# Optimization experiments

Measured on AMD Instinct MI355X. Metric: run time of the kernel, lower is better.

Reference implementation:

```python
import jax, jax.numpy as jnp
import numpy as np
import math

B, H, S, D = 2, 16, 2048, 64
MASK_NEG = -1e9


def setup_inputs() -> dict:
    key = jax.random.key(0)
    kq, kk, kv, kc, km = jax.random.split(key, 5)
    q = jax.random.normal(kq, (B, H, S, D), dtype=jnp.float32)
    k = jax.random.normal(kk, (B, H, S, D), dtype=jnp.float32)
    v = jax.random.normal(kv, (B, H, S, D), dtype=jnp.float32)
    constant = jax.random.normal(kc, (1, H, 1, 1), dtype=jnp.float32)
    mask = jax.random.randint(km, (B, S), 0, 2, dtype=jnp.int32)  # 1 = masked out
    return {"q": q, "k": k, "v": v, "constant": constant, "mask": mask}


def leaky_softmax(x, leaky_factor):
    # custom 'leaky' softmax: denominator gets an extra exp(c - max) * S term
    m = jnp.max(x, axis=-1, keepdims=True)
    exp_x = jnp.exp(x - m)
    leak = jnp.exp(leaky_factor - m) * x.shape[-1]
    return exp_x / (jnp.sum(exp_x, axis=-1, keepdims=True) + leak)


def reference(q, k, v, constant, mask):
    scale = jnp.float32(1.0 / math.sqrt(q.shape[-1]))
    # scores: [B,H,S,S]
    scores = jnp.einsum("bhqd,bhkd->bhqk", q, k) * scale
    m = mask.astype(q.dtype)[:, None, None, :]  # [B,1,1,S]
    scores = scores + m * MASK_NEG
    probs = leaky_softmax(scores, constant)
    out = jnp.einsum("bhqk,bhkd->bhqd", probs, v)
    return out, probs
```

## Files before the change

kernel.cpp:

```cpp
#include <hip/hip_runtime.h>
#include <hip/hip_bf16.h>
#include <cstdint>
#include <cstddef>

#define BB 2
#define HH 16
#define SS 2048
#define DD 64
#define NBH (BB * HH)
#define BQ 16
#define NWAVES 8
#define BLK 512
#define CW 512
#define NCHUNK (SS / CW)
#define CSTRIDE 516

typedef __attribute__((ext_vector_type(8))) short bf16x8;
typedef __attribute__((ext_vector_type(4))) float f32x4;
typedef __attribute__((ext_vector_type(4))) unsigned short us4;

#define LGKM_BAR() asm volatile("s_waitcnt lgkmcnt(0)\n\ts_barrier" ::: "memory")

__device__ __forceinline__ unsigned short f2bf(float x) {
  union { float f; uint32_t u; } c;
  c.f = x;
  uint32_t u = c.u;
  uint32_t r = (u + 0x7FFFu + ((u >> 16) & 1u)) >> 16;
  return (unsigned short)r;
}

__global__ __launch_bounds__(256) void cvt_qk_kernel(
    const float* __restrict__ q, const float* __restrict__ k,
    unsigned short* __restrict__ qb, unsigned short* __restrict__ kb) {
  size_t i = ((size_t)blockIdx.x * 256 + threadIdx.x) * 4;
  float4 a = *(const float4*)(q + i);
  float4 b = *(const float4*)(k + i);
  us4 qa = {f2bf(a.x), f2bf(a.y), f2bf(a.z), f2bf(a.w)};
  us4 ka = {f2bf(b.x), f2bf(b.y), f2bf(b.z), f2bf(b.w)};
  *(us4*)(qb + i) = qa;
  *(us4*)(kb + i) = ka;
}

__global__ __launch_bounds__(256) void cvt_vt_kernel(
    const float* __restrict__ v, unsigned short* __restrict__ vt) {
  __shared__ unsigned short t[64][65];
  const int tid = threadIdx.x;
  const int bh = blockIdx.y;
  const int s0 = blockIdx.x * 64;
  const float* vb = v + ((size_t)bh * SS + s0) * DD;
#pragma unroll
  for (int it = 0; it < 16; ++it) {
    int idx = it * 256 + tid;
    int s = idx >> 6, d = idx & 63;
    t[s][d] = f2bf(vb[idx]);
  }
  __syncthreads();
  unsigned short* vo = vt + (size_t)bh * DD * SS + s0;
#pragma unroll
  for (int it = 0; it < 4; ++it) {
    int idx = it * 256 + tid;
    int d = idx >> 4;
    int s4 = (idx & 15) * 4;
    us4 w = {t[s4 + 0][d], t[s4 + 1][d], t[s4 + 2][d], t[s4 + 3][d]};
    *(us4*)(vo + (size_t)d * SS + s4) = w;
  }
}

__global__ __launch_bounds__(BLK, 2) void attn_kernel(
    const unsigned short* __restrict__ qb,
    const unsigned short* __restrict__ kb,
    const unsigned short* __restrict__ vt,
    const float* __restrict__ cst,
    const int* __restrict__ mask,
    float* __restrict__ out,
    float* __restrict__ probs) {
  __shared__ float pch[BQ][CSTRIDE];
  __shared__ float stats[NWAVES][BQ];
  __shared__ float rowinv[BQ];

  const int tid = threadIdx.x;
  const int wave = tid >> 6;
  const int lane = tid & 63;
  const int quad = lane >> 4;
  const int l16 = lane & 15;
  const int bh = blockIdx.y;
  const int bidx = bh >> 4;
  const int h = bh & 15;
  const int q0 = blockIdx.x * BQ;

  const unsigned short* qrow = qb + ((size_t)bh * SS + q0 + l16) * DD + quad * 8;
  bf16x8 aq0 = *(const bf16x8*)(qrow);
  bf16x8 aq1 = *(const bf16x8*)(qrow + 32);

  const unsigned short* kbase = kb + (size_t)bh * SS * DD;
  f32x4 acc[16];
#pragma unroll
  for (int t = 0; t < 16; ++t) {
    int col0 = (wave + 8 * t) * 16;
    const unsigned short* krow = kbase + (size_t)(col0 + l16) * DD + quad * 8;
    bf16x8 bk0 = *(const bf16x8*)(krow);
    bf16x8 bk1 = *(const bf16x8*)(krow + 32);
    f32x4 c = {0.f, 0.f, 0.f, 0.f};
    c = __builtin_amdgcn_mfma_f32_16x16x32_bf16(aq0, bk0, c, 0, 0, 0);
    c = __builtin_amdgcn_mfma_f32_16x16x32_bf16(aq1, bk1, c, 0, 0, 0);
    acc[t] = c;
  }

  float rsum[4] = {0.f, 0.f, 0.f, 0.f};
#pragma unroll
  for (int t = 0; t < 16; ++t) {
    int col = (wave + 8 * t) * 16 + l16;
    int mk = mask[bidx * SS + col];
#pragma unroll
    for (int r = 0; r < 4; ++r) {
      float e = mk ? 0.0f : __expf(acc[t][r] * 0.125f);
      acc[t][r] = e;
      rsum[r] += e;
    }
  }
#pragma unroll
  for (int off = 8; off >= 1; off >>= 1)
#pragma unroll
    for (int r = 0; r < 4; ++r)
      rsum[r] += __shfl_xor(rsum[r], off, 64);
  if (l16 == 0)
#pragma unroll
    for (int r = 0; r < 4; ++r) stats[wave][quad * 4 + r] = rsum[r];
  __syncthreads();
  if (tid < BQ) {
    float s = 0.f;
#pragma unroll
    for (int w = 0; w < NWAVES; ++w) s += stats[w][tid];
    float denom = s + __expf(cst[h]) * (float)SS;
    rowinv[tid] = 1.0f / denom;
  }
  __syncthreads();
  float inv[4];
#pragma unroll
  for (int r = 0; r < 4; ++r) inv[r] = rowinv[quad * 4 + r];

  f32x4 acco[4];
#pragma unroll
  for (int dt = 0; dt < 4; ++dt) acco[dt] = (f32x4){0.f, 0.f, 0.f, 0.f};
  const unsigned short* vbase = vt + (size_t)bh * DD * SS;
#pragma unroll
  for (int c = 0; c < NCHUNK; ++c) {
    const int kg0 = c * CW + wave * 64 + quad * 8;
    bf16x8 v0[4];
#pragma unroll
    for (int dt = 0; dt < 4; ++dt)
      v0[dt] = *(const bf16x8*)(vbase + (size_t)(dt * 16 + l16) * SS + kg0);

    if (c) LGKM_BAR();
#pragma unroll
    for (int tt = 0; tt < 4; ++tt) {
      int t = c * 4 + tt;
      int lcol = tt * 128 + wave * 16 + l16;
#pragma unroll
      for (int r = 0; r < 4; ++r)
        pch[quad * 4 + r][lcol] = acc[t][r] * inv[r];
    }
    LGKM_BAR();

    {
      const f32x4* ap4 = (const f32x4*)&pch[l16][wave * 64 + quad * 8];
      f32x4 p0 = ap4[0], p1 = ap4[1];
      union { bf16x8 v8; uint32_t u[4]; } apu;
      asm("v_cvt_pk_bf16_f32 %0, %1, %2" : "=v"(apu.u[0]) : "v"(p0.x), "v"(p0.y));
      asm("v_cvt_pk_bf16_f32 %0, %1, %2" : "=v"(apu.u[1]) : "v"(p0.z), "v"(p0.w));
      asm("v_cvt_pk_bf16_f32 %0, %1, %2" : "=v"(apu.u[2]) : "v"(p1.x), "v"(p1.y));
      asm("v_cvt_pk_bf16_f32 %0, %1, %2" : "=v"(apu.u[3]) : "v"(p1.z), "v"(p1.w));
      bf16x8 ap = apu.v8;
      bf16x8 v1[4];
#pragma unroll
      for (int dt = 0; dt < 4; ++dt)
        v1[dt] = *(const bf16x8*)(vbase + (size_t)(dt * 16 + l16) * SS + kg0 + 32);
#pragma unroll
      for (int dt = 0; dt < 4; ++dt)
        acco[dt] = __builtin_amdgcn_mfma_f32_16x16x32_bf16(ap, v0[dt], acco[dt], 0, 0, 0);

      const f32x4* bp4 = (const f32x4*)&pch[l16][wave * 64 + 32 + quad * 8];
      f32x4 q0v = bp4[0], q1v = bp4[1];
      union { bf16x8 v8; uint32_t u[4]; } bpu;
      asm("v_cvt_pk_bf16_f32 %0, %1, %2" : "=v"(bpu.u[0]) : "v"(q0v.x), "v"(q0v.y));
      asm("v_cvt_pk_bf16_f32 %0, %1, %2" : "=v"(bpu.u[1]) : "v"(q0v.z), "v"(q0v.w));
      asm("v_cvt_pk_bf16_f32 %0, %1, %2" : "=v"(bpu.u[2]) : "v"(q1v.x), "v"(q1v.y));
      asm("v_cvt_pk_bf16_f32 %0, %1, %2" : "=v"(bpu.u[3]) : "v"(q1v.z), "v"(q1v.w));
      bf16x8 bp = bpu.v8;
#pragma unroll
      for (int dt = 0; dt < 4; ++dt)
        acco[dt] = __builtin_amdgcn_mfma_f32_16x16x32_bf16(bp, v1[dt], acco[dt], 0, 0, 0);
    }

#pragma unroll
    for (int i = 0; i < 4; ++i) {
      int f = i * BLK + tid;
      int row = f >> 7, c4 = f & 127;
      f32x4 val = *(const f32x4*)&pch[row][c4 * 4];
      f32x4* dst = (f32x4*)(probs + (size_t)bh * SS * SS +
                            (size_t)(q0 + row) * SS + c * CW) + c4;
      *dst = val;
    }
  }

  LGKM_BAR();
  float* outp = &pch[0][0];
#pragma unroll
  for (int dt = 0; dt < 4; ++dt)
#pragma unroll
    for (int r = 0; r < 4; ++r)
      outp[((wave * BQ) + quad * 4 + r) * DD + dt * 16 + l16] = acco[dt][r];
  LGKM_BAR();
  for (int e = tid; e < BQ * DD; e += BLK) {
    int row = e >> 6, col = e & 63;
    float s = 0.f;
#pragma unroll
    for (int w = 0; w < NWAVES; ++w) s += outp[(w * BQ + row) * DD + col];
    out[((size_t)bh * SS + q0 + row) * DD + col] = s;
  }
}

extern "C" void kernel_launch(void* const* d_in, const int* in_sizes, int n_in,
                              void* d_out, int out_size, void* d_ws, size_t ws_size,
                              hipStream_t stream) {
  const float* q = (const float*)d_in[0];
  const float* k = (const float*)d_in[1];
  const float* v = (const float*)d_in[2];
  const float* cst = (const float*)d_in[3];
  const int* mask = (const int*)d_in[4];

  float* out = (float*)d_out;
  float* probs = out + (size_t)NBH * SS * DD;

  const size_t nelem = (size_t)NBH * SS * DD;
  unsigned short* qb = (unsigned short*)d_ws;
  unsigned short* kb = qb + nelem;
  unsigned short* vt = kb + nelem;

  cvt_qk_kernel<<<dim3((unsigned)(nelem / (256 * 4))), 256, 0, stream>>>(q, k, qb, kb);
  cvt_vt_kernel<<<dim3(SS / 64, NBH), 256, 0, stream>>>(v, vt);

  attn_kernel<<<dim3(SS / BQ, NBH), BLK, 0, stream>>>(qb, kb, vt, cst, mask, out, probs);
}
```

Measured before the change: 849.7 us.

## Recompute QK scores instead of holding them to raise attention kernel occupancy

The attention kernel no longer keeps all 16 score tiles in registers. A first pass computes only the row sums, and a second pass recomputes the QK MFMAs and exps for each chunk. This cuts register pressure so launch bounds can move from 2 to 4 blocks per SM, at the cost of doubling the QK MFMA, K loads and exp work. Probs stores become nontemporal, and the V transpose now writes scalar elements instead of 4-wide vectors.

Measured after the change: 865.9 us. No clear change (+1.9%).

```diff
diff --git a/kernel.cpp b/kernel.cpp
--- a/kernel.cpp
+++ b/kernel.cpp
@@ -57,16 +57,14 @@
   __syncthreads();
   unsigned short* vo = vt + (size_t)bh * DD * SS + s0;
 #pragma unroll
-  for (int it = 0; it < 4; ++it) {
+  for (int it = 0; it < 16; ++it) {
     int idx = it * 256 + tid;
-    int d = idx >> 4;
-    int s4 = (idx & 15) * 4;
-    us4 w = {t[s4 + 0][d], t[s4 + 1][d], t[s4 + 2][d], t[s4 + 3][d]};
-    *(us4*)(vo + (size_t)d * SS + s4) = w;
-  }
-}
-
-__global__ __launch_bounds__(BLK, 2) void attn_kernel(
+    int d = idx >> 6, s = idx & 63;
+    vo[(size_t)d * SS + s] = t[s][d];
+  }
+}
+
+__global__ __launch_bounds__(BLK, 4) void attn_kernel(
     const unsigned short* __restrict__ qb,
     const unsigned short* __restrict__ kb,
     const unsigned short* __restrict__ vt,
@@ -93,7 +91,9 @@
   bf16x8 aq1 = *(const bf16x8*)(qrow + 32);
 
   const unsigned short* kbase = kb + (size_t)bh * SS * DD;
-  f32x4 acc[16];
+  const int* mrow = mask + bidx * SS;
+
+  float rsum[4] = {0.f, 0.f, 0.f, 0.f};
 #pragma unroll
   for (int t = 0; t < 16; ++t) {
     int col0 = (wave + 8 * t) * 16;
@@ -103,20 +103,10 @@
     f32x4 c = {0.f, 0.f, 0.f, 0.f};
     c = __builtin_amdgcn_mfma_f32_16x16x32_bf16(aq0, bk0, c, 0, 0, 0);
     c = __builtin_amdgcn_mfma_f32_16x16x32_bf16(aq1, bk1, c, 0, 0, 0);
-    acc[t] = c;
-  }
-
-  float rsum[4] = {0.f, 0.f, 0.f, 0.f};
-#pragma unroll
-  for (int t = 0; t < 16; ++t) {
-    int col = (wave + 8 * t) * 16 + l16;
-    int mk = mask[bidx * SS + col];
-#pragma unroll
-    for (int r = 0; r < 4; ++r) {
-      float e = mk ? 0.0f : __expf(acc[t][r] * 0.125f);
-      acc[t][r] = e;
-      rsum[r] += e;
-    }
+    int mk = mrow[col0 + l16];
+#pragma unroll
+    for (int r = 0; r < 4; ++r)
+      rsum[r] += mk ? 0.0f : __expf(c[r] * 0.125f);
   }
 #pragma unroll
   for (int off = 8; off >= 1; off >>= 1)
@@ -155,10 +145,20 @@
 #pragma unroll
     for (int tt = 0; tt < 4; ++tt) {
       int t = c * 4 + tt;
+      int col0 = (wave + 8 * t) * 16;
+      const unsigned short* krow = kbase + (size_t)(col0 + l16) * DD + quad * 8;
+      bf16x8 bk0 = *(const bf16x8*)(krow);
+      bf16x8 bk1 = *(const bf16x8*)(krow + 32);
+      f32x4 ct = {0.f, 0.f, 0.f, 0.f};
+      ct = __builtin_amdgcn_mfma_f32_16x16x32_bf16(aq0, bk0, ct, 0, 0, 0);
+      ct = __builtin_amdgcn_mfma_f32_16x16x32_bf16(aq1, bk1, ct, 0, 0, 0);
+      int mk = mrow[col0 + l16];
       int lcol = tt * 128 + wave * 16 + l16;
 #pragma unroll
-      for (int r = 0; r < 4; ++r)
-        pch[quad * 4 + r][lcol] = acc[t][r] * inv[r];
+      for (int r = 0; r < 4; ++r) {
+        float e = mk ? 0.0f : __expf(ct[r] * 0.125f) * inv[r];
+        pch[quad * 4 + r][lcol] = e;
+      }
     }
     LGKM_BAR();
 
@@ -199,7 +199,7 @@
       f32x4 val = *(const f32x4*)&pch[row][c4 * 4];
       f32x4* dst = (f32x4*)(probs + (size_t)bh * SS * SS +
                             (size_t)(q0 + row) * SS + c * CW) + c4;
-      *dst = val;
+      __builtin_nontemporal_store(val, dst);
     }
   }
 
```
